# Kernel optimization log

Hardware: AMD Instinct MI355X
Metric: run time of the kernel (lower is better)

The kernel has to match this reference:

```python
import jax, jax.numpy as jnp
import numpy as np

VOCAB, EMB = 32000, 300
B, T, S = 64, 25, 50
NF = 100
FS = (3, 4, 5)
H = 256
OUT = 31


def setup_inputs() -> dict:
    key = jax.random.key(0)
    ks = jax.random.split(key, 12)
    inp = {}
    inp["dialogue"] = jax.random.randint(ks[0], (B, T, S), 0, VOCAB)
    inp["emb"] = jax.random.normal(ks[1], (VOCAB, EMB), jnp.float32) * 0.1
    for j, fs in enumerate(FS):
        inp[f"conv_w{fs}"] = jax.random.normal(ks[2 + j], (NF, 1, fs, EMB), jnp.float32) * (1.0 / np.sqrt(fs * EMB))
        inp[f"conv_b{fs}"] = jnp.zeros((NF,), jnp.float32)
    IN = NF * len(FS)
    sc = 1.0 / np.sqrt(H)
    inp["wih"] = jax.random.normal(ks[5], (4 * H, IN), jnp.float32) * sc
    inp["whh"] = jax.random.normal(ks[6], (4 * H, H), jnp.float32) * sc
    inp["bih"] = jnp.zeros((4 * H,), jnp.float32)
    inp["bhh"] = jnp.zeros((4 * H,), jnp.float32)
    inp["wih_r"] = jax.random.normal(ks[7], (4 * H, IN), jnp.float32) * sc
    inp["whh_r"] = jax.random.normal(ks[8], (4 * H, H), jnp.float32) * sc
    inp["bih_r"] = jnp.zeros((4 * H,), jnp.float32)
    inp["bhh_r"] = jnp.zeros((4 * H,), jnp.float32)
    inp["h2o_w"] = jax.random.normal(ks[9], (OUT, 2 * H), jnp.float32) * sc
    inp["h2o_b"] = jnp.zeros((OUT,), jnp.float32)
    return inp


def _cnn_embed(tokens, emb, conv_params):
    # tokens: [B,T,S] int -> per-utterance CNN features [B,T, NF*len(FS)]
    x = emb[tokens.reshape(-1, S)]           # [B*T, S, EMB] embedding lookup
    x = x[:, None, :, :]                      # NCHW: [B*T, 1, S, EMB]
    feats = []
    for (w, b) in conv_params:
        c = jax.lax.conv_general_dilated(
            x, w, (1, 1), 'VALID', dimension_numbers=('NCHW', 'OIHW', 'NCHW'))
        c = jax.nn.relu(c + b[None, :, None, None])   # [B*T, NF, S-fs+1, 1]
        feats.append(jnp.max(c[..., 0], axis=2))      # max-pool over time -> [B*T, NF]
    return jnp.concatenate(feats, axis=1).reshape(B, T, -1)


def _lstm(x, wih, whh, bih, bhh):
    # single-layer LSTM, torch gate order (i, f, g, o); x: [B,Tm,I] -> [B,Tm,H]
    h0 = jnp.zeros((x.shape[0], H), x.dtype)

    def step(carry, xt):
        h, c = carry
        g = xt @ wih.T + h @ whh.T + bih + bhh        # [B, 4H]
        i, f, gg, o = jnp.split(g, 4, axis=-1)
        c = jax.nn.sigmoid(f) * c + jax.nn.sigmoid(i) * jnp.tanh(gg)
        h = jax.nn.sigmoid(o) * jnp.tanh(c)
        return (h, c), h

    _, hs = jax.lax.scan(step, (h0, h0), jnp.swapaxes(x, 0, 1))
    return jnp.swapaxes(hs, 0, 1)


def reference(dialogue, emb, conv_w3, conv_b3, conv_w4, conv_b4, conv_w5, conv_b5,
              wih, whh, bih, bhh, wih_r, whh_r, bih_r, bhh_r, h2o_w, h2o_b):
    r_in = _cnn_embed(dialogue, emb,
                      [(conv_w3, conv_b3), (conv_w4, conv_b4), (conv_w5, conv_b5)])
    # bi=True branch: self.rnn consumes the sequence in reverse order, outputs
    # stored back at their original positions == reverse, scan, reverse.
    rev = _lstm(r_in[:, ::-1], wih, whh, bih, bhh)[:, ::-1]
    # rnn_r consumes the sequence forward (teacher_forcing_ratio=None path)
    fwd = _lstm(r_in, wih_r, whh_r, bih_r, bhh_r)
    h = jnp.concatenate([rev, fwd], axis=-1)          # [B,T,2H]
    return jax.nn.sigmoid(h @ h2o_w.T + h2o_b)        # [B,T,OUT]
```

## Files before the change

kernel.cpp:

```cpp
#include <hip/hip_runtime.h>
#include <hip/hip_bf16.h>

#define NB 64
#define NT 25
#define NS 50
#define EMBD 300
#define NFILT 100
#define HD 256
#define NOUT 31
#define NBT (NB*NT)

#define KP3 928
#define KP4 1216
#define KP5 1504
#define XS_LEN 15104

typedef unsigned short ush;
typedef __attribute__((ext_vector_type(8))) short short8;
typedef __attribute__((ext_vector_type(4))) float f32x4;

__device__ __forceinline__ float hsum4(float4 a) { return (a.x + a.y) + (a.z + a.w); }
__device__ __forceinline__ void fma4(float4& a, float4 w, float4 x) {
    a.x = fmaf(w.x, x.x, a.x); a.y = fmaf(w.y, x.y, a.y);
    a.z = fmaf(w.z, x.z, a.z); a.w = fmaf(w.w, x.w, a.w);
}
__device__ __forceinline__ float sigmoidf_(float x) { return 1.0f / (1.0f + __expf(-x)); }
__device__ __forceinline__ float tanh_fast(float x) {
    x = fminf(fmaxf(x, -15.0f), 15.0f);
    const float e = __expf(2.0f * x);
    return (e - 1.0f) / (e + 1.0f);
}

__device__ __forceinline__ ush f2bf(float f) {
    union { float f; unsigned u; } v; v.f = f;
    unsigned r = v.u + 0x7FFF + ((v.u >> 16) & 1);
    return (ush)(r >> 16);
}

__device__ __forceinline__ short8 ld8_a8(const ush* p) {
    short8 r;
    ((uint2*)&r)[0] = *(const uint2*)p;
    ((uint2*)&r)[1] = *(const uint2*)(p + 4);
    return r;
}

__device__ __forceinline__ void gload_lds16u(const ush* g, ush* l) {
    __builtin_amdgcn_global_load_lds(
        (const __attribute__((address_space(1))) unsigned int*)g,
        (__attribute__((address_space(3))) unsigned int*)l, 16, 0, 0);
}

__global__ __launch_bounds__(256) void k_prep(
    const float* __restrict__ w3, const float* __restrict__ w4, const float* __restrict__ w5,
    ush* __restrict__ wb)
{
    const int S0 = 112 * KP3, S1 = S0 + 112 * KP4, S2 = S1 + 112 * KP5;
    int idx = blockIdx.x * 256 + threadIdx.x;
    if (idx >= S2) return;
    int rel, Kp, K; const float* src;
    if (idx < S0)      { rel = idx;      Kp = KP3; K = 900;  src = w3; }
    else if (idx < S1) { rel = idx - S0; Kp = KP4; K = 1200; src = w4; }
    else               { rel = idx - S1; Kp = KP5; K = 1500; src = w5; }
    int f = rel / Kp, k = rel - f * Kp;
    float v = (f < NFILT && k < K) ? src[(size_t)f * K + k] : 0.0f;
    wb[idx] = f2bf(v);
}

__global__ __launch_bounds__(256) void k_prep2(
    const float* __restrict__ whh, const float* __restrict__ whh_r,
    ush* __restrict__ wb2)
{
    const int idx = blockIdx.x * 256 + threadIdx.x;
    const int dir = idx >> 18;
    const int rem = idx & 262143;
    const int n = rem >> 8, k = rem & 255;
    const int j = n >> 2, gate = n & 3;
    const float* src = dir ? whh_r : whh;
    const float v = src[(size_t)(gate * 256 + j) * 256 + k];
    const int w = n >> 7, r = n & 127;
    const int nt = r >> 4, l15 = r & 15;
    const int kk = k >> 5, kg = (k >> 3) & 3, e = k & 7;
    const int lane8 = (kg * 16 + l15) * 8 + e;
    size_t dst = (size_t)(dir * 8 + w) * 32768;
    if (nt < 4) dst += nt * 4096 + kk * 512 + lane8;
    else        dst += 16384 + kk * 2048 + (nt - 4) * 512 + lane8;
    wb2[dst] = f2bf(v);
}

__global__ __launch_bounds__(512) void k_conv(
    const int* __restrict__ tok, const float* __restrict__ emb,
    const ush* __restrict__ wb,
    const float* __restrict__ b3, const float* __restrict__ b4, const float* __restrict__ b5,
    float* __restrict__ rin)
{
    __shared__ ush xs[2][XS_LEN];
    const int bt0 = blockIdx.x * 2;
    const int tid = threadIdx.x;
    for (int i4 = tid; i4 < 2 * NS * 75; i4 += 512) {
        const int smp = i4 / (NS * 75);
        const int rem = i4 - smp * (NS * 75);
        const int s = rem / 75, e4 = rem - s * 75;
        const int t = tok[(bt0 + smp) * NS + s];
        float4 v = ((const float4*)(emb + (size_t)t * EMBD))[e4];
        uint2 pk;
        pk.x = (unsigned)f2bf(v.x) | ((unsigned)f2bf(v.y) << 16);
        pk.y = (unsigned)f2bf(v.z) | ((unsigned)f2bf(v.w) << 16);
        *(uint2*)(&xs[smp][s * 300 + e4 * 4]) = pk;
    }
    for (int i = NS * EMBD + tid; i < XS_LEN; i += 512) { xs[0][i] = 0; xs[1][i] = 0; }
    __syncthreads();

    const int wave = tid >> 6, lane = tid & 63;
    const int col = lane & 15, kg = lane >> 4;

    for (int job = wave; job < 21; job += 8) {
        const int fsi = job / 7, ntile = job - fsi * 7;
        int Kp, P, obase; const ush* W; const float* bias;
        if (fsi == 0)      { Kp = KP3; P = 48; W = wb;                       bias = b3; obase = 0; }
        else if (fsi == 1) { Kp = KP4; P = 47; W = wb + 112 * KP3;           bias = b4; obase = NFILT; }
        else               { Kp = KP5; P = 46; W = wb + 112 * (KP3 + KP4);   bias = b5; obase = 2 * NFILT; }

        const ush* wrow = W + (size_t)(ntile * 16 + col) * Kp + kg * 8;
        const ush* xb0 = &xs[0][col * 300 + kg * 8];
        const ush* xb1 = &xs[1][col * 300 + kg * 8];
        f32x4 a00 = {0,0,0,0}, a01 = {0,0,0,0}, a02 = {0,0,0,0};
        f32x4 a10 = {0,0,0,0}, a11 = {0,0,0,0}, a12 = {0,0,0,0};

        const int nks = Kp / 32;
        short8 wr0 = *(const short8*)(wrow);
        short8 wr1 = *(const short8*)(wrow + 32);
        for (int ks = 0; ks < nks; ++ks) {
            const int k0 = ks * 32;
            short8 bfrag = wr0;
            wr0 = wr1;
            if (ks + 2 < nks) wr1 = *(const short8*)(wrow + k0 + 64);
            short8 p0 = ld8_a8(xb0 + k0);
            short8 p1 = ld8_a8(xb0 + 16 * 300 + k0);
            short8 p2 = ld8_a8(xb0 + 32 * 300 + k0);
            short8 q0 = ld8_a8(xb1 + k0);
            short8 q1 = ld8_a8(xb1 + 16 * 300 + k0);
            short8 q2 = ld8_a8(xb1 + 32 * 300 + k0);
            a00 = __builtin_amdgcn_mfma_f32_16x16x32_bf16(p0, bfrag, a00, 0, 0, 0);
            a01 = __builtin_amdgcn_mfma_f32_16x16x32_bf16(p1, bfrag, a01, 0, 0, 0);
            a02 = __builtin_amdgcn_mfma_f32_16x16x32_bf16(p2, bfrag, a02, 0, 0, 0);
            a10 = __builtin_amdgcn_mfma_f32_16x16x32_bf16(q0, bfrag, a10, 0, 0, 0);
            a11 = __builtin_amdgcn_mfma_f32_16x16x32_bf16(q1, bfrag, a11, 0, 0, 0);
            a12 = __builtin_amdgcn_mfma_f32_16x16x32_bf16(q2, bfrag, a12, 0, 0, 0);
        }

        float pm0 = -1e30f, pm1 = -1e30f;
        #pragma unroll
        for (int reg = 0; reg < 4; ++reg) {
            pm0 = fmaxf(pm0, a00[reg]); pm0 = fmaxf(pm0, a01[reg]);
            pm1 = fmaxf(pm1, a10[reg]); pm1 = fmaxf(pm1, a11[reg]);
            const int r2 = 32 + kg * 4 + reg;
            if (r2 < P) { pm0 = fmaxf(pm0, a02[reg]); pm1 = fmaxf(pm1, a12[reg]); }
        }
        pm0 = fmaxf(pm0, __shfl_xor(pm0, 16, 64));
        pm0 = fmaxf(pm0, __shfl_xor(pm0, 32, 64));
        pm1 = fmaxf(pm1, __shfl_xor(pm1, 16, 64));
        pm1 = fmaxf(pm1, __shfl_xor(pm1, 32, 64));
        if (lane < 16) {
            const int f = ntile * 16 + lane;
            if (f < NFILT) {
                const float bb = bias[f];
                rin[(size_t)bt0 * (3 * NFILT) + obase + f]       = fmaxf(0.0f, pm0 + bb);
                rin[(size_t)(bt0 + 1) * (3 * NFILT) + obase + f] = fmaxf(0.0f, pm1 + bb);
            }
        }
    }
}

__global__ __launch_bounds__(256) void k_gin(
    const float* __restrict__ rin,
    const float* __restrict__ wih,   const float* __restrict__ bih,   const float* __restrict__ bhh,
    const float* __restrict__ wih_r, const float* __restrict__ bih_r, const float* __restrict__ bhh_r,
    float* __restrict__ gin)
{
    __shared__ float xsh[8 * EMBD];
    const int bt0 = blockIdx.x * 8;
    const int tid = threadIdx.x;
    const float4* src = (const float4*)(rin + (size_t)bt0 * EMBD);
    for (int i4 = tid; i4 < 8 * EMBD / 4; i4 += 256) ((float4*)xsh)[i4] = src[i4];
    __syncthreads();
    for (int g2 = tid; g2 < 2 * 1024; g2 += 256) {
        const int d = g2 >> 10;
        const int g = g2 & 1023;
        const float* wp = (d ? wih_r : wih) + (size_t)g * EMBD;
        const float bb = d ? (bih_r[g] + bhh_r[g]) : (bih[g] + bhh[g]);
        const float4* w4p = (const float4*)wp;
        float4 acc[8];
        #pragma unroll
        for (int r = 0; r < 8; ++r) acc[r] = {0,0,0,0};
        for (int k = 0; k < EMBD / 4; ++k) {
            const float4 wv = w4p[k];
            #pragma unroll
            for (int r = 0; r < 8; ++r) fma4(acc[r], wv, ((const float4*)(xsh + r * EMBD))[k]);
        }
        const int gp = ((g & 255) << 2) | (g >> 8);
        #pragma unroll
        for (int r = 0; r < 8; ++r) {
            const int bt = bt0 + r;
            const int b = bt / NT, t = bt - b * NT;
            gin[(((size_t)d * NT + t) * NB + b) * 1024 + gp] = hsum4(acc[r]) + bb;
        }
    }
}

__global__ __launch_bounds__(512, 1) void k_lstm(
    const float* __restrict__ gin,
    const ush* __restrict__ wb2,
    float* __restrict__ hs)
{
    const int bid = blockIdx.x;
    const int dir = bid >> 2, bq = bid & 3;
    const int tid = threadIdx.x;
    const int wave = tid >> 6, lane = tid & 63;
    const int l15 = lane & 15, kg = lane >> 4;
    const int m = l15 & 3, quad = l15 >> 2;

    __shared__ __align__(16) ush hb[2][16 * 264];
    __shared__ __align__(16) ush wring[8][2][2048];

    for (int i = tid; i < 16 * 264; i += 512) hb[0][i] = 0;

    const ush* wbase = wb2 + (size_t)(dir * 8 + wave) * 32768;
    const ush* wstr = wbase + 16384;
    const float* gb = gin + (size_t)dir * (NT * NB * 1024);
    float* hsb = hs + (size_t)dir * NBT * HD;

    short8 wpa[4][8];
    #pragma unroll
    for (int nt = 0; nt < 4; ++nt)
        #pragma unroll
        for (int kk = 0; kk < 8; ++kk)
            wpa[nt][kk] = *(const short8*)(wbase + nt * 4096 + kk * 512 + lane * 8);
    __syncthreads();

    const int b_row = kg * 4 + m;
    const int bglob = bq * 16 + b_row;

    float c[8] = {0.f,0.f,0.f,0.f,0.f,0.f,0.f,0.f};

    for (int s = 0; s < NT; ++s) {
        const int t = dir ? s : (NT - 1 - s);
        const ush* hc = hb[s & 1];
        ush* hn = hb[(s + 1) & 1];

        float4 gxr[8];
        #pragma unroll
        for (int nt = 0; nt < 8; ++nt) {
            const int j_g = wave * 32 + nt * 4 + quad;
            gxr[nt] = *(const float4*)(gb + (((size_t)t * NB + bglob) << 10) + j_g * 4);
        }

        #pragma unroll
        for (int q = 0; q < 4; ++q)
            gload_lds16u(wstr + 0 * 2048 + q * 512 + lane * 8, &wring[wave][0][q * 512]);
        #pragma unroll
        for (int q = 0; q < 4; ++q)
            gload_lds16u(wstr + 1 * 2048 + q * 512 + lane * 8, &wring[wave][1][q * 512]);

        f32x4 acc[8];
        #pragma unroll
        for (int nt = 0; nt < 8; ++nt) acc[nt] = (f32x4){0.f, 0.f, 0.f, 0.f};

        #pragma unroll
        for (int kk = 0; kk < 8; ++kk) {
            if (kk < 7) asm volatile("s_waitcnt vmcnt(4)" ::: "memory");
            else        asm volatile("s_waitcnt vmcnt(0)" ::: "memory");
            __builtin_amdgcn_sched_barrier(0);
            const short8 av = *(const short8*)(hc + l15 * 264 + kk * 32 + kg * 8);
            #pragma unroll
            for (int nt = 0; nt < 4; ++nt)
                acc[nt] = __builtin_amdgcn_mfma_f32_16x16x32_bf16(av, wpa[nt][kk], acc[nt], 0, 0, 0);
            #pragma unroll
            for (int q = 0; q < 4; ++q) {
                const short8 bbf = *(const short8*)(&wring[wave][kk & 1][q * 512 + lane * 8]);
                acc[4 + q] = __builtin_amdgcn_mfma_f32_16x16x32_bf16(av, bbf, acc[4 + q], 0, 0, 0);
            }
            if (kk < 6) {
                asm volatile("s_waitcnt lgkmcnt(0)" ::: "memory");
                __builtin_amdgcn_sched_barrier(0);
                #pragma unroll
                for (int q = 0; q < 4; ++q)
                    gload_lds16u(wstr + (size_t)(kk + 2) * 2048 + q * 512 + lane * 8,
                                 &wring[wave][kk & 1][q * 512]);
            }
        }

        #pragma unroll
        for (int nt = 0; nt < 8; ++nt) {
            float r0 = acc[nt][0], r1 = acc[nt][1], r2 = acc[nt][2], r3 = acc[nt][3];
            { float x = (m & 1) ? r0 : r1; x = __shfl_xor(x, 1, 64); if (m & 1) r0 = x; else r1 = x; }
            { float x = (m & 1) ? r2 : r3; x = __shfl_xor(x, 1, 64); if (m & 1) r2 = x; else r3 = x; }
            { float x = (m & 2) ? r0 : r2; x = __shfl_xor(x, 2, 64); if (m & 2) r0 = x; else r2 = x; }
            { float x = (m & 2) ? r1 : r3; x = __shfl_xor(x, 2, 64); if (m & 2) r1 = x; else r3 = x; }
            const float4 gx = gxr[nt];
            const float vi = sigmoidf_(r0 + gx.x);
            const float vf = sigmoidf_(r1 + gx.y);
            const float vg = tanh_fast(r2 + gx.z);
            const float vo = sigmoidf_(r3 + gx.w);
            const float cc = vf * c[nt] + vi * vg;
            c[nt] = cc;
            const float hh = vo * tanh_fast(cc);
            const int j_g = wave * 32 + nt * 4 + quad;
            hn[b_row * 264 + j_g] = f2bf(hh);
            hsb[((size_t)bglob * NT + t) * HD + j_g] = hh;
        }
        __syncthreads();
    }
}

__global__ __launch_bounds__(64) void k_out(
    const float* __restrict__ hs, const float* __restrict__ w, const float* __restrict__ bias,
    float* __restrict__ out)
{
    __shared__ float hsh[2 * HD];
    const int bt = blockIdx.x;
    const int tid = threadIdx.x;
    const float4* rev4 = (const float4*)(hs + (size_t)bt * HD);
    const float4* fwd4 = (const float4*)(hs + ((size_t)NBT + bt) * HD);
    for (int i = tid; i < 2 * HD / 4; i += 64)
        ((float4*)hsh)[i] = (i < HD / 4) ? rev4[i] : fwd4[i - HD / 4];
    __syncthreads();
    if (tid < NOUT) {
        const float4* wr = (const float4*)(w + (size_t)tid * (2 * HD));
        float4 acc{0,0,0,0};
        for (int k = 0; k < 2 * HD / 4; ++k) fma4(acc, wr[k], ((const float4*)hsh)[k]);
        out[(size_t)bt * NOUT + tid] = sigmoidf_(hsum4(acc) + bias[tid]);
    }
}

extern "C" void kernel_launch(void* const* d_in, const int* in_sizes, int n_in,
                              void* d_out, int out_size, void* d_ws, size_t ws_size,
                              hipStream_t stream)
{
    const int*   tok   = (const int*)d_in[0];
    const float* emb   = (const float*)d_in[1];
    const float* w3    = (const float*)d_in[2];
    const float* b3    = (const float*)d_in[3];
    const float* w4    = (const float*)d_in[4];
    const float* b4    = (const float*)d_in[5];
    const float* w5    = (const float*)d_in[6];
    const float* b5    = (const float*)d_in[7];
    const float* wih   = (const float*)d_in[8];
    const float* whh   = (const float*)d_in[9];
    const float* bih   = (const float*)d_in[10];
    const float* bhh   = (const float*)d_in[11];
    const float* wih_r = (const float*)d_in[12];
    const float* whh_r = (const float*)d_in[13];
    const float* bih_r = (const float*)d_in[14];
    const float* bhh_r = (const float*)d_in[15];
    const float* h2o_w = (const float*)d_in[16];
    const float* h2o_b = (const float*)d_in[17];

    float* ws  = (float*)d_ws;
    float* rin = ws;
    float* gin = rin + (size_t)NBT * 3 * NFILT;
    float* hs  = gin + (size_t)2 * NBT * 1024;
    ush* wb  = (ush*)gin;
    ush* wb2 = (ush*)rin;

    k_prep <<<1596, 256, 0, stream>>>(w3, w4, w5, wb);
    k_conv <<<NBT / 2, 512, 0, stream>>>(tok, emb, wb, b3, b4, b5, rin);
    k_gin  <<<NBT / 8, 256, 0, stream>>>(rin, wih, bih, bhh, wih_r, bih_r, bhh_r, gin);
    k_prep2<<<2048, 256, 0, stream>>>(whh, whh_r, wb2);
    k_lstm <<<8, 512, 0, stream>>>(gin, wb2, hs);
    k_out  <<<NBT, 64, 0, stream>>>(hs, h2o_w, h2o_b, (float*)d_out);
}
```

Baseline: 485.6 us.

## Split LSTM hidden dim across blocks with global h exchange and flag sync

The LSTM kernel changes from partitioning the batch across 4 blocks per direction, where each block streamed half of W_hh through LDS every step, to partitioning the hidden units across 4 blocks. Each block now keeps its full W_hh slice resident in registers and computes all 64 batch rows. The new hidden state is exchanged through global memory, with per-step atomic flags acting as an inter-block barrier. This removes the per-step weight streaming, at the cost of a global-memory round trip and a spin-wait between cooperating blocks every timestep, plus an extra memset.

```diff
diff --git a/kernel.cpp b/kernel.cpp
--- a/kernel.cpp
+++ b/kernel.cpp
@@ -42,12 +42,6 @@
     ((uint2*)&r)[0] = *(const uint2*)p;
     ((uint2*)&r)[1] = *(const uint2*)(p + 4);
     return r;
-}
-
-__device__ __forceinline__ void gload_lds16u(const ush* g, ush* l) {
-    __builtin_amdgcn_global_load_lds(
-        (const __attribute__((address_space(1))) unsigned int*)g,
-        (__attribute__((address_space(3))) unsigned int*)l, 16, 0, 0);
 }
 
 __global__ __launch_bounds__(256) void k_prep(
@@ -77,13 +71,10 @@
     const int j = n >> 2, gate = n & 3;
     const float* src = dir ? whh_r : whh;
     const float v = src[(size_t)(gate * 256 + j) * 256 + k];
-    const int w = n >> 7, r = n & 127;
-    const int nt = r >> 4, l15 = r & 15;
+    const int wg = n >> 8, wv = (n >> 6) & 3, nt = (n >> 4) & 3, l15 = n & 15;
     const int kk = k >> 5, kg = (k >> 3) & 3, e = k & 7;
-    const int lane8 = (kg * 16 + l15) * 8 + e;
-    size_t dst = (size_t)(dir * 8 + w) * 32768;
-    if (nt < 4) dst += nt * 4096 + kk * 512 + lane8;
-    else        dst += 16384 + kk * 2048 + (nt - 4) * 512 + lane8;
+    const size_t dst = (size_t)((dir * 4 + wg) * 4 + wv) * 16384
+                     + (nt * 8 + kk) * 512 + (kg * 16 + l15) * 8 + e;
     wb2[dst] = f2bf(v);
 }
 
@@ -207,108 +198,103 @@
     }
 }
 
-__global__ __launch_bounds__(512, 1) void k_lstm(
+__global__ __launch_bounds__(256, 1) void k_lstm(
     const float* __restrict__ gin,
     const ush* __restrict__ wb2,
+    ush* __restrict__ hg,
+    unsigned* __restrict__ flags,
     float* __restrict__ hs)
 {
     const int bid = blockIdx.x;
-    const int dir = bid >> 2, bq = bid & 3;
+    const int dir = bid >> 2, wg = bid & 3;
     const int tid = threadIdx.x;
     const int wave = tid >> 6, lane = tid & 63;
     const int l15 = lane & 15, kg = lane >> 4;
     const int m = l15 & 3, quad = l15 >> 2;
 
-    __shared__ __align__(16) ush hb[2][16 * 264];
-    __shared__ __align__(16) ush wring[8][2][2048];
-
-    for (int i = tid; i < 16 * 264; i += 512) hb[0][i] = 0;
-
-    const ush* wbase = wb2 + (size_t)(dir * 8 + wave) * 32768;
-    const ush* wstr = wbase + 16384;
+    short8 wreg[4][8];
+    {
+        const ush* wbase = wb2 + (size_t)((dir * 4 + wg) * 4 + wave) * 16384;
+        #pragma unroll
+        for (int nt = 0; nt < 4; ++nt)
+            #pragma unroll
+            for (int kk = 0; kk < 8; ++kk)
+                wreg[nt][kk] = *(const short8*)(wbase + (nt * 8 + kk) * 512 + lane * 8);
+    }
+
     const float* gb = gin + (size_t)dir * (NT * NB * 1024);
     float* hsb = hs + (size_t)dir * NBT * HD;
-
-    short8 wpa[4][8];
+    ush* hgd = hg + dir * (2 * 4 * 4096);
+    unsigned* flg = flags + dir * 64;
+
+    float c[16];
     #pragma unroll
-    for (int nt = 0; nt < 4; ++nt)
-        #pragma unroll
-        for (int kk = 0; kk < 8; ++kk)
-            wpa[nt][kk] = *(const short8*)(wbase + nt * 4096 + kk * 512 + lane * 8);
-    __syncthreads();
-
-    const int b_row = kg * 4 + m;
-    const int bglob = bq * 16 + b_row;
-
-    float c[8] = {0.f,0.f,0.f,0.f,0.f,0.f,0.f,0.f};
+    for (int q = 0; q < 16; ++q) c[q] = 0.0f;
 
     for (int s = 0; s < NT; ++s) {
         const int t = dir ? s : (NT - 1 - s);
-        const ush* hc = hb[s & 1];
-        ush* hn = hb[(s + 1) & 1];
-
-        float4 gxr[8];
-        #pragma unroll
-        for (int nt = 0; nt < 8; ++nt) {
-            const int j_g = wave * 32 + nt * 4 + quad;
-            gxr[nt] = *(const float4*)(gb + (((size_t)t * NB + bglob) << 10) + j_g * 4);
-        }
-
-        #pragma unroll
-        for (int q = 0; q < 4; ++q)
-            gload_lds16u(wstr + 0 * 2048 + q * 512 + lane * 8, &wring[wave][0][q * 512]);
-        #pragma unroll
-        for (int q = 0; q < 4; ++q)
-            gload_lds16u(wstr + 1 * 2048 + q * 512 + lane * 8, &wring[wave][1][q * 512]);
-
-        f32x4 acc[8];
-        #pragma unroll
-        for (int nt = 0; nt < 8; ++nt) acc[nt] = (f32x4){0.f, 0.f, 0.f, 0.f};
+        const ush* hcur = hgd + (s & 1) * (4 * 4096);
+        ush* hnxt = hgd + ((s + 1) & 1) * (4 * 4096);
+
+        if (s > 0) {
+            if (tid < 4) {
+                while (atomicAdd(&flg[tid * 16], 0u) < (unsigned)s)
+                    __builtin_amdgcn_s_sleep(2);
+            }
+            __syncthreads();
+            __threadfence();
+        }
+
+        f32x4 acc[4][4];
+        #pragma unroll
+        for (int mt = 0; mt < 4; ++mt)
+            #pragma unroll
+            for (int nt = 0; nt < 4; ++nt) acc[mt][nt] = (f32x4){0.f, 0.f, 0.f, 0.f};
 
         #pragma unroll
         for (int kk = 0; kk < 8; ++kk) {
-            if (kk < 7) asm volatile("s_waitcnt vmcnt(4)" ::: "memory");
-            else        asm volatile("s_waitcnt vmcnt(0)" ::: "memory");
-            __builtin_amdgcn_sched_barrier(0);
-            const short8 av = *(const short8*)(hc + l15 * 264 + kk * 32 + kg * 8);
-            #pragma unroll
-            for (int nt = 0; nt < 4; ++nt)
-                acc[nt] = __builtin_amdgcn_mfma_f32_16x16x32_bf16(av, wpa[nt][kk], acc[nt], 0, 0, 0);
-            #pragma unroll
-            for (int q = 0; q < 4; ++q) {
-                const short8 bbf = *(const short8*)(&wring[wave][kk & 1][q * 512 + lane * 8]);
-                acc[4 + q] = __builtin_amdgcn_mfma_f32_16x16x32_bf16(av, bbf, acc[4 + q], 0, 0, 0);
+            const ush* hsl = hcur + (kk >> 1) * 4096 + (kk & 1) * 32 + kg * 8;
+            short8 av0 = *(const short8*)(hsl + (0 * 16 + l15) * 64);
+            short8 av1 = *(const short8*)(hsl + (1 * 16 + l15) * 64);
+            short8 av2 = *(const short8*)(hsl + (2 * 16 + l15) * 64);
+            short8 av3 = *(const short8*)(hsl + (3 * 16 + l15) * 64);
+            #pragma unroll
+            for (int nt = 0; nt < 4; ++nt) {
+                acc[0][nt] = __builtin_amdgcn_mfma_f32_16x16x32_bf16(av0, wreg[nt][kk], acc[0][nt], 0, 0, 0);
+                acc[1][nt] = __builtin_amdgcn_mfma_f32_16x16x32_bf16(av1, wreg[nt][kk], acc[1][nt], 0, 0, 0);
+                acc[2][nt] = __builtin_amdgcn_mfma_f32_16x16x32_bf16(av2, wreg[nt][kk], acc[2][nt], 0, 0, 0);
+                acc[3][nt] = __builtin_amdgcn_mfma_f32_16x16x32_bf16(av3, wreg[nt][kk], acc[3][nt], 0, 0, 0);
             }
-            if (kk < 6) {
-                asm volatile("s_waitcnt lgkmcnt(0)" ::: "memory");
-                __builtin_amdgcn_sched_barrier(0);
-                #pragma unroll
-                for (int q = 0; q < 4; ++q)
-                    gload_lds16u(wstr + (size_t)(kk + 2) * 2048 + q * 512 + lane * 8,
-                                 &wring[wave][kk & 1][q * 512]);
+        }
+
+        #pragma unroll
+        for (int mt = 0; mt < 4; ++mt) {
+            const int b = mt * 16 + kg * 4 + m;
+            #pragma unroll
+            for (int nt = 0; nt < 4; ++nt) {
+                float r0 = acc[mt][nt][0], r1 = acc[mt][nt][1], r2 = acc[mt][nt][2], r3 = acc[mt][nt][3];
+                { float x = (m & 1) ? r0 : r1; x = __shfl_xor(x, 1, 64); if (m & 1) r0 = x; else r1 = x; }
+                { float x = (m & 1) ? r2 : r3; x = __shfl_xor(x, 1, 64); if (m & 1) r2 = x; else r3 = x; }
+                { float x = (m & 2) ? r0 : r2; x = __shfl_xor(x, 2, 64); if (m & 2) r0 = x; else r2 = x; }
+                { float x = (m & 2) ? r1 : r3; x = __shfl_xor(x, 2, 64); if (m & 2) r1 = x; else r3 = x; }
+                const int jl = wave * 16 + nt * 4 + quad;
+                const int jg = wg * 64 + jl;
+                const float4 gx = *(const float4*)(gb + (((size_t)t * NB + b) << 10) + jg * 4);
+                const float vi = sigmoidf_(r0 + gx.x);
+                const float vf = sigmoidf_(r1 + gx.y);
+                const float vg = tanh_fast(r2 + gx.z);
+                const float vo = sigmoidf_(r3 + gx.w);
+                const float cc = vf * c[mt * 4 + nt] + vi * vg;
+                c[mt * 4 + nt] = cc;
+                const float hh = vo * tanh_fast(cc);
+                hnxt[wg * 4096 + b * 64 + jl] = f2bf(hh);
+                hsb[((size_t)b * NT + t) * HD + jg] = hh;
             }
         }
 
-        #pragma unroll
-        for (int nt = 0; nt < 8; ++nt) {
-            float r0 = acc[nt][0], r1 = acc[nt][1], r2 = acc[nt][2], r3 = acc[nt][3];
-            { float x = (m & 1) ? r0 : r1; x = __shfl_xor(x, 1, 64); if (m & 1) r0 = x; else r1 = x; }
-            { float x = (m & 1) ? r2 : r3; x = __shfl_xor(x, 1, 64); if (m & 1) r2 = x; else r3 = x; }
-            { float x = (m & 2) ? r0 : r2; x = __shfl_xor(x, 2, 64); if (m & 2) r0 = x; else r2 = x; }
-            { float x = (m & 2) ? r1 : r3; x = __shfl_xor(x, 2, 64); if (m & 2) r1 = x; else r3 = x; }
-            const float4 gx = gxr[nt];
-            const float vi = sigmoidf_(r0 + gx.x);
-            const float vf = sigmoidf_(r1 + gx.y);
-            const float vg = tanh_fast(r2 + gx.z);
-            const float vo = sigmoidf_(r3 + gx.w);
-            const float cc = vf * c[nt] + vi * vg;
-            c[nt] = cc;
-            const float hh = vo * tanh_fast(cc);
-            const int j_g = wave * 32 + nt * 4 + quad;
-            hn[b_row * 264 + j_g] = f2bf(hh);
-            hsb[((size_t)bglob * NT + t) * HD + j_g] = hh;
-        }
+        __threadfence();
         __syncthreads();
+        if (tid == 0) atomicExch(&flg[wg * 16], (unsigned)(s + 1));
     }
 }
 
@@ -361,11 +347,14 @@
     float* hs  = gin + (size_t)2 * NBT * 1024;
     ush* wb  = (ush*)gin;
     ush* wb2 = (ush*)rin;
+    ush* hg  = (ush*)(rin + 262144);
+    unsigned* flags = (unsigned*)(rin + 262144 + 32768);
 
     k_prep <<<1596, 256, 0, stream>>>(w3, w4, w5, wb);
     k_conv <<<NBT / 2, 512, 0, stream>>>(tok, emb, wb, b3, b4, b5, rin);
     k_gin  <<<NBT / 8, 256, 0, stream>>>(rin, wih, bih, bhh, wih_r, bih_r, bhh_r, gin);
     k_prep2<<<2048, 256, 0, stream>>>(whh, whh_r, wb2);
-    k_lstm <<<8, 512, 0, stream>>>(gin, wb2, hs);
+    hipMemsetAsync(hg, 0, 65536 * sizeof(ush) + 128 * sizeof(unsigned), stream);
+    k_lstm <<<8, 256, 0, stream>>>(gin, wb2, hg, flags, hs);
     k_out  <<<NBT, 64, 0, stream>>>(hs, h2o_w, h2o_b, (float*)d_out);
 }
```

New measurement: 525.8 us. +8.3%, slower.

## Halve LSTM block to 4 waves, each owning 16 gate tiles with LDS-resident weights

Applied to the files above, without the earlier changes.

The recurrent LSTM kernel now runs 4 waves per block instead of 8, so each wave computes 64 hidden units (16 MFMA N-tiles). Six tiles of W_hh stay in registers, two more are preloaded once into LDS, and the remaining eight are streamed from global memory into a double-buffered LDS ring on every step. The weight pre-pack layout is changed to match. The aim is to cut per-step barrier and wave-coordination cost and to keep more of the weights on-chip. The trade-off is more serial MFMA work and more streamed weight traffic per wave on the latency-bound recurrence.

```diff
diff --git a/kernel.cpp b/kernel.cpp
--- a/kernel.cpp
+++ b/kernel.cpp
@@ -77,13 +77,10 @@
     const int j = n >> 2, gate = n & 3;
     const float* src = dir ? whh_r : whh;
     const float v = src[(size_t)(gate * 256 + j) * 256 + k];
-    const int w = n >> 7, r = n & 127;
-    const int nt = r >> 4, l15 = r & 15;
+    const int wave = n >> 8, nt = (n >> 4) & 15, l15 = n & 15;
     const int kk = k >> 5, kg = (k >> 3) & 3, e = k & 7;
-    const int lane8 = (kg * 16 + l15) * 8 + e;
-    size_t dst = (size_t)(dir * 8 + w) * 32768;
-    if (nt < 4) dst += nt * 4096 + kk * 512 + lane8;
-    else        dst += 16384 + kk * 2048 + (nt - 4) * 512 + lane8;
+    const size_t dst = ((size_t)((dir * 4 + wave) * 16 + nt)) * 4096
+                     + kk * 512 + (kg * 16 + l15) * 8 + e;
     wb2[dst] = f2bf(v);
 }
 
@@ -207,7 +204,7 @@
     }
 }
 
-__global__ __launch_bounds__(512, 1) void k_lstm(
+__global__ __launch_bounds__(256, 1) void k_lstm(
     const float* __restrict__ gin,
     const ush* __restrict__ wb2,
     float* __restrict__ hs)
@@ -220,77 +217,89 @@
     const int m = l15 & 3, quad = l15 >> 2;
 
     __shared__ __align__(16) ush hb[2][16 * 264];
-    __shared__ __align__(16) ush wring[8][2][2048];
-
-    for (int i = tid; i < 16 * 264; i += 512) hb[0][i] = 0;
-
-    const ush* wbase = wb2 + (size_t)(dir * 8 + wave) * 32768;
-    const ush* wstr = wbase + 16384;
+    __shared__ __align__(16) ush wldsP[4][2][8][512];
+    __shared__ __align__(16) ush wring[4][2][8][512];
+
+    for (int i = tid; i < 16 * 264; i += 256) hb[0][i] = 0;
+
+    const ush* wbase = wb2 + (size_t)(dir * 4 + wave) * 65536;
     const float* gb = gin + (size_t)dir * (NT * NB * 1024);
     float* hsb = hs + (size_t)dir * NBT * HD;
 
-    short8 wpa[4][8];
+    short8 wreg[6][8];
     #pragma unroll
-    for (int nt = 0; nt < 4; ++nt)
+    for (int nt = 0; nt < 6; ++nt)
         #pragma unroll
         for (int kk = 0; kk < 8; ++kk)
-            wpa[nt][kk] = *(const short8*)(wbase + nt * 4096 + kk * 512 + lane * 8);
+            wreg[nt][kk] = *(const short8*)(wbase + nt * 4096 + kk * 512 + lane * 8);
+    #pragma unroll
+    for (int p = 0; p < 2; ++p)
+        #pragma unroll
+        for (int kk = 0; kk < 8; ++kk)
+            gload_lds16u(wbase + (6 + p) * 4096 + kk * 512 + lane * 8, &wldsP[wave][p][kk][0]);
+    asm volatile("s_waitcnt vmcnt(0)" ::: "memory");
     __syncthreads();
 
     const int b_row = kg * 4 + m;
     const int bglob = bq * 16 + b_row;
 
-    float c[8] = {0.f,0.f,0.f,0.f,0.f,0.f,0.f,0.f};
+    float c[16];
+    #pragma unroll
+    for (int q = 0; q < 16; ++q) c[q] = 0.0f;
 
     for (int s = 0; s < NT; ++s) {
         const int t = dir ? s : (NT - 1 - s);
         const ush* hc = hb[s & 1];
         ush* hn = hb[(s + 1) & 1];
 
-        float4 gxr[8];
-        #pragma unroll
-        for (int nt = 0; nt < 8; ++nt) {
-            const int j_g = wave * 32 + nt * 4 + quad;
-            gxr[nt] = *(const float4*)(gb + (((size_t)t * NB + bglob) << 10) + j_g * 4);
-        }
-
-        #pragma unroll
-        for (int q = 0; q < 4; ++q)
-            gload_lds16u(wstr + 0 * 2048 + q * 512 + lane * 8, &wring[wave][0][q * 512]);
-        #pragma unroll
-        for (int q = 0; q < 4; ++q)
-            gload_lds16u(wstr + 1 * 2048 + q * 512 + lane * 8, &wring[wave][1][q * 512]);
-
-        f32x4 acc[8];
-        #pragma unroll
-        for (int nt = 0; nt < 8; ++nt) acc[nt] = (f32x4){0.f, 0.f, 0.f, 0.f};
+        float4 gxr[16];
+        #pragma unroll
+        for (int nt = 0; nt < 16; ++nt)
+            gxr[nt] = *(const float4*)(gb + (((size_t)t * NB + bglob) << 10)
+                                       + wave * 256 + nt * 16 + quad * 4);
+
+        #pragma unroll
+        for (int q = 0; q < 8; ++q)
+            gload_lds16u(wbase + (8 + q) * 4096 + 0 * 512 + lane * 8, &wring[wave][0][q][0]);
+        #pragma unroll
+        for (int q = 0; q < 8; ++q)
+            gload_lds16u(wbase + (8 + q) * 4096 + 1 * 512 + lane * 8, &wring[wave][1][q][0]);
+
+        f32x4 acc[16];
+        #pragma unroll
+        for (int nt = 0; nt < 16; ++nt) acc[nt] = (f32x4){0.f, 0.f, 0.f, 0.f};
 
         #pragma unroll
         for (int kk = 0; kk < 8; ++kk) {
-            if (kk < 7) asm volatile("s_waitcnt vmcnt(4)" ::: "memory");
+            if (kk < 7) asm volatile("s_waitcnt vmcnt(8)" ::: "memory");
             else        asm volatile("s_waitcnt vmcnt(0)" ::: "memory");
             __builtin_amdgcn_sched_barrier(0);
             const short8 av = *(const short8*)(hc + l15 * 264 + kk * 32 + kg * 8);
             #pragma unroll
-            for (int nt = 0; nt < 4; ++nt)
-                acc[nt] = __builtin_amdgcn_mfma_f32_16x16x32_bf16(av, wpa[nt][kk], acc[nt], 0, 0, 0);
+            for (int nt = 0; nt < 6; ++nt)
+                acc[nt] = __builtin_amdgcn_mfma_f32_16x16x32_bf16(av, wreg[nt][kk], acc[nt], 0, 0, 0);
             #pragma unroll
-            for (int q = 0; q < 4; ++q) {
-                const short8 bbf = *(const short8*)(&wring[wave][kk & 1][q * 512 + lane * 8]);
-                acc[4 + q] = __builtin_amdgcn_mfma_f32_16x16x32_bf16(av, bbf, acc[4 + q], 0, 0, 0);
+            for (int p = 0; p < 2; ++p) {
+                const short8 bbf = *(const short8*)(&wldsP[wave][p][kk][lane * 8]);
+                acc[6 + p] = __builtin_amdgcn_mfma_f32_16x16x32_bf16(av, bbf, acc[6 + p], 0, 0, 0);
+            }
+            #pragma unroll
+            for (int q = 0; q < 8; ++q) {
+                const short8 bbf = *(const short8*)(&wring[wave][kk & 1][q][lane * 8]);
+                acc[8 + q] = __builtin_amdgcn_mfma_f32_16x16x32_bf16(av, bbf, acc[8 + q], 0, 0, 0);
             }
             if (kk < 6) {
                 asm volatile("s_waitcnt lgkmcnt(0)" ::: "memory");
                 __builtin_amdgcn_sched_barrier(0);
                 #pragma unroll
-                for (int q = 0; q < 4; ++q)
-                    gload_lds16u(wstr + (size_t)(kk + 2) * 2048 + q * 512 + lane * 8,
-                                 &wring[wave][kk & 1][q * 512]);
+                for (int q = 0; q < 8; ++q)
+                    gload_lds16u(wbase + (8 + q) * 4096 + (kk + 2) * 512 + lane * 8,
+                                 &wring[wave][kk & 1][q][0]);
             }
         }
 
         #pragma unroll
-        for (int nt = 0; nt < 8; ++nt) {
+        for (int nt = 0; nt < 16; ++nt) {
             float r0 = acc[nt][0], r1 = acc[nt][1], r2 = acc[nt][2], r3 = acc[nt][3];
             { float x = (m & 1) ? r0 : r1; x = __shfl_xor(x, 1, 64); if (m & 1) r0 = x; else r1 = x; }
             { float x = (m & 1) ? r2 : r3; x = __shfl_xor(x, 1, 64); if (m & 1) r2 = x; else r3 = x; }
@@ -304,7 +313,7 @@
             const float cc = vf * c[nt] + vi * vg;
             c[nt] = cc;
             const float hh = vo * tanh_fast(cc);
-            const int j_g = wave * 32 + nt * 4 + quad;
+            const int j_g = wave * 64 + nt * 4 + quad;
             hn[b_row * 264 + j_g] = f2bf(hh);
             hsb[((size_t)bglob * NT + t) * HD + j_g] = hh;
         }
@@ -366,6 +375,6 @@
     k_conv <<<NBT / 2, 512, 0, stream>>>(tok, emb, wb, b3, b4, b5, rin);
     k_gin  <<<NBT / 8, 256, 0, stream>>>(rin, wih, bih, bhh, wih_r, bih_r, bhh_r, gin);
     k_prep2<<<2048, 256, 0, stream>>>(whh, whh_r, wb2);
-    k_lstm <<<8, 512, 0, stream>>>(gin, wb2, hs);
+    k_lstm <<<8, 256, 0, stream>>>(gin, wb2, hs);
     k_out  <<<NBT, 64, 0, stream>>>(hs, h2o_w, h2o_b, (float*)d_out);
 }
```

After: 532.5 us. 9.7% more time.

## Batch four utterances per conv block and stream all LSTM weights via swizzled LDS

Applied to the files above, without the earlier changes.

The conv kernel now handles four utterances per block instead of two, so each weight fragment loaded from global memory feeds twice as many MFMAs, at the cost of twice the LDS footprint (about 121 KB) and more accumulator registers. The LSTM kernel no longer keeps half of the recurrent weights resident in registers. It streams all eight n-tiles per k-slice through a double-buffered LDS ring, with an XOR-swizzled layout written by k_prep2 to avoid bank conflicts. This frees many VGPRs but doubles the per-step global-to-LDS traffic on the serial recurrence path.

```diff
diff --git a/kernel.cpp b/kernel.cpp
--- a/kernel.cpp
+++ b/kernel.cpp
@@ -78,12 +78,9 @@
     const float* src = dir ? whh_r : whh;
     const float v = src[(size_t)(gate * 256 + j) * 256 + k];
     const int w = n >> 7, r = n & 127;
-    const int nt = r >> 4, l15 = r & 15;
     const int kk = k >> 5, kg = (k >> 3) & 3, e = k & 7;
-    const int lane8 = (kg * 16 + l15) * 8 + e;
-    size_t dst = (size_t)(dir * 8 + w) * 32768;
-    if (nt < 4) dst += nt * 4096 + kk * 512 + lane8;
-    else        dst += 16384 + kk * 2048 + (nt - 4) * 512 + lane8;
+    const size_t dst = ((size_t)(dir * 8 + w) * 8 + kk) * 4096
+                     + r * 32 + ((kg ^ ((r >> 1) & 3)) * 8) + e;
     wb2[dst] = f2bf(v);
 }
 
@@ -93,10 +90,10 @@
     const float* __restrict__ b3, const float* __restrict__ b4, const float* __restrict__ b5,
     float* __restrict__ rin)
 {
-    __shared__ ush xs[2][XS_LEN];
-    const int bt0 = blockIdx.x * 2;
+    __shared__ ush xs[4][XS_LEN];
+    const int bt0 = blockIdx.x * 4;
     const int tid = threadIdx.x;
-    for (int i4 = tid; i4 < 2 * NS * 75; i4 += 512) {
+    for (int i4 = tid; i4 < 4 * NS * 75; i4 += 512) {
         const int smp = i4 / (NS * 75);
         const int rem = i4 - smp * (NS * 75);
         const int s = rem / 75, e4 = rem - s * 75;
@@ -107,7 +104,9 @@
         pk.y = (unsigned)f2bf(v.z) | ((unsigned)f2bf(v.w) << 16);
         *(uint2*)(&xs[smp][s * 300 + e4 * 4]) = pk;
     }
-    for (int i = NS * EMBD + tid; i < XS_LEN; i += 512) { xs[0][i] = 0; xs[1][i] = 0; }
+    for (int i = NS * EMBD + tid; i < XS_LEN; i += 512) {
+        xs[0][i] = 0; xs[1][i] = 0; xs[2][i] = 0; xs[3][i] = 0;
+    }
     __syncthreads();
 
     const int wave = tid >> 6, lane = tid & 63;
@@ -121,10 +120,11 @@
         else               { Kp = KP5; P = 46; W = wb + 112 * (KP3 + KP4);   bias = b5; obase = 2 * NFILT; }
 
         const ush* wrow = W + (size_t)(ntile * 16 + col) * Kp + kg * 8;
-        const ush* xb0 = &xs[0][col * 300 + kg * 8];
-        const ush* xb1 = &xs[1][col * 300 + kg * 8];
-        f32x4 a00 = {0,0,0,0}, a01 = {0,0,0,0}, a02 = {0,0,0,0};
-        f32x4 a10 = {0,0,0,0}, a11 = {0,0,0,0}, a12 = {0,0,0,0};
+        f32x4 acc[4][3];
+        #pragma unroll
+        for (int smp = 0; smp < 4; ++smp)
+            #pragma unroll
+            for (int pt = 0; pt < 3; ++pt) acc[smp][pt] = (f32x4){0.f, 0.f, 0.f, 0.f};
 
         const int nks = Kp / 32;
         short8 wr0 = *(const short8*)(wrow);
@@ -134,38 +134,34 @@
             short8 bfrag = wr0;
             wr0 = wr1;
             if (ks + 2 < nks) wr1 = *(const short8*)(wrow + k0 + 64);
-            short8 p0 = ld8_a8(xb0 + k0);
-            short8 p1 = ld8_a8(xb0 + 16 * 300 + k0);
-            short8 p2 = ld8_a8(xb0 + 32 * 300 + k0);
-            short8 q0 = ld8_a8(xb1 + k0);
-            short8 q1 = ld8_a8(xb1 + 16 * 300 + k0);
-            short8 q2 = ld8_a8(xb1 + 32 * 300 + k0);
-            a00 = __builtin_amdgcn_mfma_f32_16x16x32_bf16(p0, bfrag, a00, 0, 0, 0);
-            a01 = __builtin_amdgcn_mfma_f32_16x16x32_bf16(p1, bfrag, a01, 0, 0, 0);
-            a02 = __builtin_amdgcn_mfma_f32_16x16x32_bf16(p2, bfrag, a02, 0, 0, 0);
-            a10 = __builtin_amdgcn_mfma_f32_16x16x32_bf16(q0, bfrag, a10, 0, 0, 0);
-            a11 = __builtin_amdgcn_mfma_f32_16x16x32_bf16(q1, bfrag, a11, 0, 0, 0);
-            a12 = __builtin_amdgcn_mfma_f32_16x16x32_bf16(q2, bfrag, a12, 0, 0, 0);
-        }
-
-        float pm0 = -1e30f, pm1 = -1e30f;
-        #pragma unroll
-        for (int reg = 0; reg < 4; ++reg) {
-            pm0 = fmaxf(pm0, a00[reg]); pm0 = fmaxf(pm0, a01[reg]);
-            pm1 = fmaxf(pm1, a10[reg]); pm1 = fmaxf(pm1, a11[reg]);
-            const int r2 = 32 + kg * 4 + reg;
-            if (r2 < P) { pm0 = fmaxf(pm0, a02[reg]); pm1 = fmaxf(pm1, a12[reg]); }
-        }
-        pm0 = fmaxf(pm0, __shfl_xor(pm0, 16, 64));
-        pm0 = fmaxf(pm0, __shfl_xor(pm0, 32, 64));
-        pm1 = fmaxf(pm1, __shfl_xor(pm1, 16, 64));
-        pm1 = fmaxf(pm1, __shfl_xor(pm1, 32, 64));
-        if (lane < 16) {
-            const int f = ntile * 16 + lane;
-            if (f < NFILT) {
-                const float bb = bias[f];
-                rin[(size_t)bt0 * (3 * NFILT) + obase + f]       = fmaxf(0.0f, pm0 + bb);
-                rin[(size_t)(bt0 + 1) * (3 * NFILT) + obase + f] = fmaxf(0.0f, pm1 + bb);
+            #pragma unroll
+            for (int smp = 0; smp < 4; ++smp) {
+                const ush* xb = &xs[smp][col * 300 + kg * 8];
+                short8 a0 = ld8_a8(xb + k0);
+                short8 a1 = ld8_a8(xb + 16 * 300 + k0);
+                short8 a2 = ld8_a8(xb + 32 * 300 + k0);
+                acc[smp][0] = __builtin_amdgcn_mfma_f32_16x16x32_bf16(a0, bfrag, acc[smp][0], 0, 0, 0);
+                acc[smp][1] = __builtin_amdgcn_mfma_f32_16x16x32_bf16(a1, bfrag, acc[smp][1], 0, 0, 0);
+                acc[smp][2] = __builtin_amdgcn_mfma_f32_16x16x32_bf16(a2, bfrag, acc[smp][2], 0, 0, 0);
+            }
+        }
+
+        #pragma unroll
+        for (int smp = 0; smp < 4; ++smp) {
+            float pm = -1e30f;
+            #pragma unroll
+            for (int reg = 0; reg < 4; ++reg) {
+                pm = fmaxf(pm, acc[smp][0][reg]);
+                pm = fmaxf(pm, acc[smp][1][reg]);
+                const int r2 = 32 + kg * 4 + reg;
+                if (r2 < P) pm = fmaxf(pm, acc[smp][2][reg]);
+            }
+            pm = fmaxf(pm, __shfl_xor(pm, 16, 64));
+            pm = fmaxf(pm, __shfl_xor(pm, 32, 64));
+            if (lane < 16) {
+                const int f = ntile * 16 + lane;
+                if (f < NFILT)
+                    rin[(size_t)(bt0 + smp) * (3 * NFILT) + obase + f] = fmaxf(0.0f, pm + bias[f]);
             }
         }
     }
@@ -219,23 +215,18 @@
     const int l15 = lane & 15, kg = lane >> 4;
     const int m = l15 & 3, quad = l15 >> 2;
 
+    __shared__ __align__(16) ush wring[8][2][4096];
     __shared__ __align__(16) ush hb[2][16 * 264];
-    __shared__ __align__(16) ush wring[8][2][2048];
 
     for (int i = tid; i < 16 * 264; i += 512) hb[0][i] = 0;
-
-    const ush* wbase = wb2 + (size_t)(dir * 8 + wave) * 32768;
-    const ush* wstr = wbase + 16384;
+    __syncthreads();
+
+    const ush* wsrc = wb2 + ((size_t)(dir * 8 + wave) * 8) * 4096;
+    ush* wd0 = &wring[wave][0][0];
+    ush* wd1 = &wring[wave][1][0];
+
     const float* gb = gin + (size_t)dir * (NT * NB * 1024);
     float* hsb = hs + (size_t)dir * NBT * HD;
-
-    short8 wpa[4][8];
-    #pragma unroll
-    for (int nt = 0; nt < 4; ++nt)
-        #pragma unroll
-        for (int kk = 0; kk < 8; ++kk)
-            wpa[nt][kk] = *(const short8*)(wbase + nt * 4096 + kk * 512 + lane * 8);
-    __syncthreads();
 
     const int b_row = kg * 4 + m;
     const int bglob = bq * 16 + b_row;
@@ -253,13 +244,10 @@
             const int j_g = wave * 32 + nt * 4 + quad;
             gxr[nt] = *(const float4*)(gb + (((size_t)t * NB + bglob) << 10) + j_g * 4);
         }
-
-        #pragma unroll
-        for (int q = 0; q < 4; ++q)
-            gload_lds16u(wstr + 0 * 2048 + q * 512 + lane * 8, &wring[wave][0][q * 512]);
-        #pragma unroll
-        for (int q = 0; q < 4; ++q)
-            gload_lds16u(wstr + 1 * 2048 + q * 512 + lane * 8, &wring[wave][1][q * 512]);
+        #pragma unroll
+        for (int i = 0; i < 8; ++i) gload_lds16u(wsrc + i * 512 + lane * 8, wd0 + i * 512);
+        #pragma unroll
+        for (int i = 0; i < 8; ++i) gload_lds16u(wsrc + 4096 + i * 512 + lane * 8, wd1 + i * 512);
 
         f32x4 acc[8];
         #pragma unroll
@@ -267,25 +255,23 @@
 
         #pragma unroll
         for (int kk = 0; kk < 8; ++kk) {
-            if (kk < 7) asm volatile("s_waitcnt vmcnt(4)" ::: "memory");
+            if (kk < 7) asm volatile("s_waitcnt vmcnt(8)" ::: "memory");
             else        asm volatile("s_waitcnt vmcnt(0)" ::: "memory");
             __builtin_amdgcn_sched_barrier(0);
+            const ush* wt = (kk & 1) ? wd1 : wd0;
             const short8 av = *(const short8*)(hc + l15 * 264 + kk * 32 + kg * 8);
             #pragma unroll
-            for (int nt = 0; nt < 4; ++nt)
-                acc[nt] = __builtin_amdgcn_mfma_f32_16x16x32_bf16(av, wpa[nt][kk], acc[nt], 0, 0, 0);
-            #pragma unroll
-            for (int q = 0; q < 4; ++q) {
-                const short8 bbf = *(const short8*)(&wring[wave][kk & 1][q * 512 + lane * 8]);
-                acc[4 + q] = __builtin_amdgcn_mfma_f32_16x16x32_bf16(av, bbf, acc[4 + q], 0, 0, 0);
-            }
-            if (kk < 6) {
+            for (int nt = 0; nt < 8; ++nt) {
+                const int row = nt * 16 + l15;
+                const short8 bbf = *(const short8*)(wt + row * 32 + ((kg ^ ((row >> 1) & 3)) * 8));
+                acc[nt] = __builtin_amdgcn_mfma_f32_16x16x32_bf16(av, bbf, acc[nt], 0, 0, 0);
+            }
+            if (kk + 2 < 8) {
                 asm volatile("s_waitcnt lgkmcnt(0)" ::: "memory");
-                __builtin_amdgcn_sched_barrier(0);
+                ush* wref = (kk & 1) ? wd1 : wd0;
                 #pragma unroll
-                for (int q = 0; q < 4; ++q)
-                    gload_lds16u(wstr + (size_t)(kk + 2) * 2048 + q * 512 + lane * 8,
-                                 &wring[wave][kk & 1][q * 512]);
+                for (int i = 0; i < 8; ++i)
+                    gload_lds16u(wsrc + (kk + 2) * 4096 + i * 512 + lane * 8, wref + i * 512);
             }
         }
 
@@ -363,7 +349,7 @@
     ush* wb2 = (ush*)rin;
 
     k_prep <<<1596, 256, 0, stream>>>(w3, w4, w5, wb);
-    k_conv <<<NBT / 2, 512, 0, stream>>>(tok, emb, wb, b3, b4, b5, rin);
+    k_conv <<<NBT / 4, 512, 0, stream>>>(tok, emb, wb, b3, b4, b5, rin);
     k_gin  <<<NBT / 8, 256, 0, stream>>>(rin, wih, bih, bhh, wih_r, bih_r, bhh_r, gin);
     k_prep2<<<2048, 256, 0, stream>>>(whh, whh_r, wb2);
     k_lstm <<<8, 512, 0, stream>>>(gin, wb2, hs);
```

Result: slower. 496.6 us (+2.3%).
